# Kernel optimization log

Measured on AMD Instinct MI355X. Metric: run time of the kernel, lower is better.

Reference implementation:

```python
import jax, jax.numpy as jnp
import numpy as np

NUM_ITERS = 3
NUM_CAPSULES = 10
NUM_ROUTES = 1152  # 32*6*6
IN_CH = 16
OUT_CH = 32
BATCH = 128


def _squash(t):
    # Faithful to original squash(tensor) with default dim=1 (the batch axis here).
    n2 = jnp.sum(t * t, axis=1, keepdims=True)
    return (n2 / (1.0 + n2)) * t / jnp.sqrt(n2)


def setup_inputs() -> dict:
    key = jax.random.key(0)
    k1, k2 = jax.random.split(key)
    x = jax.random.normal(k1, (BATCH, NUM_ROUTES, IN_CH), dtype=jnp.float32)
    route_weights = jax.random.normal(
        k2, (NUM_CAPSULES, NUM_ROUTES, IN_CH, OUT_CH), dtype=jnp.float32)
    return {"x": x, "route_weights": route_weights}


def reference(x, route_weights):
    # prediction vectors u_hat: [C, B, R, O]
    pred = jnp.einsum('bri,crio->cbro', x, route_weights)
    logits = jnp.zeros_like(pred)  # [C, B, R, O], matching torch zeros of pred size
    outputs = None
    for i in range(NUM_ITERS):
        # routing_softmax with dim=2 -> softmax over the routes axis
        c = jax.nn.softmax(logits, axis=2)
        s = jnp.sum(c * pred, axis=2, keepdims=True)  # [C, B, 1, O]
        outputs = _squash(s)
        if i != NUM_ITERS - 1:
            # delta logits: [C, B, R, 1], broadcasts over O when added
            logits = logits + jnp.sum(pred * outputs, axis=-1, keepdims=True)
    # match torch output shape [C, B, 1, 1, O]
    return outputs[:, :, :, None, :]
```

## Files before the change

### kernel.cpp

```cpp
#include <hip/hip_runtime.h>
#include <math.h>

#define NB 128
#define NR 1152
#define NC 10
#define NCHK 24

typedef __attribute__((ext_vector_type(8))) short bf16x8;
typedef __attribute__((ext_vector_type(16))) float f32x16;

__device__ __forceinline__ unsigned pk_bf16(float a, float b) {
    unsigned r;
    asm("v_cvt_pk_bf16_f32 %0, %1, %2" : "=v"(r) : "v"(a), "v"(b));
    return r;
}

template<int MODE>
__global__ __launch_bounds__(512, 2) void pass_g(const float* __restrict__ x,
                                                 const float* __restrict__ W,
                                                 const float* __restrict__ oacc,
                                                 float* __restrict__ part_s,
                                                 float* __restrict__ pZ)
{
    __shared__ float lds[16384];
    const int pb = blockIdx.x;
    const int lin = (pb & 7) * 30 + (pb >> 3);
    const int rch = lin / 10;
    const int c   = lin - rch * 10;
    const int t = threadIdx.x;
    const int w = t >> 6, l = t & 63;
    const int h = w >> 1, bp = w & 1;
    const int lo5 = l & 31, hi1 = l >> 5;
    const int r0 = rch * 48 + h * 12;

    if (MODE == 1) {
        const float* ob = oacc + (size_t)c * NB * 32;
        for (int idx = t; idx < 4096; idx += 512)
            lds[(idx >> 5) * 33 + (idx & 31)] = ob[idx];
    }
    __syncthreads();

    float ov0[16], ov1[16];
    if (MODE == 1) {
#pragma unroll
        for (int j = 0; j < 16; ++j) {
            int orow = (j & 3) + 8 * (j >> 2) + 4 * hi1;
            ov0[j] = lds[(bp * 64 + lo5) * 33 + orow];
            ov1[j] = lds[(bp * 64 + 32 + lo5) * 33 + orow];
        }
    }

    f32x16 acc0, acc1, zz;
#pragma unroll
    for (int j = 0; j < 16; ++j) { acc0[j] = 0.f; acc1[j] = 0.f; zz[j] = 0.f; }
    float Z0 = 0.f, Z1 = 0.f;

    const float* wb  = W + ((size_t)(c * NR + r0) * 16 + hi1 * 8) * 32 + lo5;
    const float* xp0 = x + ((size_t)(bp * 64 + lo5) * NR + r0) * 16 + hi1 * 8;
    const float* xp1 = x + ((size_t)(bp * 64 + 32 + lo5) * NR + r0) * 16 + hi1 * 8;

    for (int rr = 0; rr < 12; ++rr) {
        float wv[8];
#pragma unroll
        for (int j = 0; j < 8; ++j) wv[j] = wb[(size_t)rr * 512 + j * 32];
        union { unsigned u[4]; bf16x8 v; } Ah, Al, Xh0, Xl0, Xh1, Xl1;
#pragma unroll
        for (int j = 0; j < 4; ++j) Ah.u[j] = pk_bf16(wv[2*j], wv[2*j+1]);
#pragma unroll
        for (int j = 0; j < 4; ++j) {
            float g0 = __uint_as_float(Ah.u[j] << 16);
            float g1 = __uint_as_float(Ah.u[j] & 0xffff0000u);
            Al.u[j] = pk_bf16(wv[2*j] - g0, wv[2*j+1] - g1);
        }
        float4 u0 = *(const float4*)(xp0 + rr * 16);
        float4 u1 = *(const float4*)(xp0 + rr * 16 + 4);
        float xv0[8] = {u0.x,u0.y,u0.z,u0.w, u1.x,u1.y,u1.z,u1.w};
#pragma unroll
        for (int j = 0; j < 4; ++j) Xh0.u[j] = pk_bf16(xv0[2*j], xv0[2*j+1]);
#pragma unroll
        for (int j = 0; j < 4; ++j) {
            float g0 = __uint_as_float(Xh0.u[j] << 16);
            float g1 = __uint_as_float(Xh0.u[j] & 0xffff0000u);
            Xl0.u[j] = pk_bf16(xv0[2*j] - g0, xv0[2*j+1] - g1);
        }
        float4 v0 = *(const float4*)(xp1 + rr * 16);
        float4 v1 = *(const float4*)(xp1 + rr * 16 + 4);
        float xv1[8] = {v0.x,v0.y,v0.z,v0.w, v1.x,v1.y,v1.z,v1.w};
#pragma unroll
        for (int j = 0; j < 4; ++j) Xh1.u[j] = pk_bf16(xv1[2*j], xv1[2*j+1]);
#pragma unroll
        for (int j = 0; j < 4; ++j) {
            float g0 = __uint_as_float(Xh1.u[j] << 16);
            float g1 = __uint_as_float(Xh1.u[j] & 0xffff0000u);
            Xl1.u[j] = pk_bf16(xv1[2*j] - g0, xv1[2*j+1] - g1);
        }

        if (MODE == 0) {
            acc0 = __builtin_amdgcn_mfma_f32_32x32x16_bf16(Ah.v, Xh0.v, acc0, 0, 0, 0);
            acc0 = __builtin_amdgcn_mfma_f32_32x32x16_bf16(Al.v, Xh0.v, acc0, 0, 0, 0);
            acc0 = __builtin_amdgcn_mfma_f32_32x32x16_bf16(Ah.v, Xl0.v, acc0, 0, 0, 0);
            acc1 = __builtin_amdgcn_mfma_f32_32x32x16_bf16(Ah.v, Xh1.v, acc1, 0, 0, 0);
            acc1 = __builtin_amdgcn_mfma_f32_32x32x16_bf16(Al.v, Xh1.v, acc1, 0, 0, 0);
            acc1 = __builtin_amdgcn_mfma_f32_32x32x16_bf16(Ah.v, Xl1.v, acc1, 0, 0, 0);
        } else {
            f32x16 q0, q1;
            q0 = __builtin_amdgcn_mfma_f32_32x32x16_bf16(Ah.v, Xh0.v, zz, 0, 0, 0);
            q1 = __builtin_amdgcn_mfma_f32_32x32x16_bf16(Ah.v, Xh1.v, zz, 0, 0, 0);
            q0 = __builtin_amdgcn_mfma_f32_32x32x16_bf16(Al.v, Xh0.v, q0, 0, 0, 0);
            q1 = __builtin_amdgcn_mfma_f32_32x32x16_bf16(Al.v, Xh1.v, q1, 0, 0, 0);
            q0 = __builtin_amdgcn_mfma_f32_32x32x16_bf16(Ah.v, Xl0.v, q0, 0, 0, 0);
            q1 = __builtin_amdgcn_mfma_f32_32x32x16_bf16(Ah.v, Xl1.v, q1, 0, 0, 0);
            float d0 = 0.f, d1 = 0.f;
#pragma unroll
            for (int j = 0; j < 16; ++j) {
                d0 = fmaf(q0[j], ov0[j], d0);
                d1 = fmaf(q1[j], ov1[j], d1);
            }
            d0 += __shfl_xor(d0, 32);
            d1 += __shfl_xor(d1, 32);
            float e0 = __expf(d0 - 20.0f);
            float e1 = __expf(d1 - 20.0f);
            Z0 += e0; Z1 += e1;
#pragma unroll
            for (int j = 0; j < 16; ++j) {
                acc0[j] = fmaf(e0, q0[j], acc0[j]);
                acc1[j] = fmaf(e1, q1[j], acc1[j]);
            }
        }
    }

    const int b0 = bp * 64 + lo5, b1 = b0 + 32;
    __syncthreads();
#pragma unroll
    for (int j = 0; j < 16; ++j) {
        int orow = (j & 3) + 8 * (j >> 2) + 4 * hi1;
        lds[h * 4096 + b0 * 32 + (orow ^ lo5)] = acc0[j];
        lds[h * 4096 + b1 * 32 + (orow ^ lo5)] = acc1[j];
    }
    __syncthreads();
    float* po = part_s + (size_t)(c * NCHK + rch) * 4096;
    for (int idx = t; idx < 4096; idx += 512) {
        int b = idx >> 5, o = idx & 31;
        float s = 0.f;
#pragma unroll
        for (int hh = 0; hh < 4; ++hh)
            s += lds[hh * 4096 + b * 32 + (o ^ (b & 31))];
        po[idx] = s;
    }
    if (MODE == 1) {
        __syncthreads();
        if (l < 32) {
            lds[h * 128 + bp * 64 + lo5] = Z0;
            lds[h * 128 + bp * 64 + 32 + lo5] = Z1;
        }
        __syncthreads();
        if (t < 128) {
            float z = lds[t] + lds[128 + t] + lds[256 + t] + lds[384 + t];
            pZ[(size_t)(c * NCHK + rch) * 128 + t] = z;
        }
    }
}

template<int MODE>
__global__ __launch_bounds__(256) void msq_k(const float* __restrict__ part_s,
                                             const float* __restrict__ pZ,
                                             float* __restrict__ oacc,
                                             float* __restrict__ dout)
{
    const int c = blockIdx.x, og = blockIdx.y;
    const int t = threadIdx.x;
    const int o_off = t & 7, b_lo = t >> 3;
    const int o = og * 8 + o_off;

    float sv[4];
    float pn = 0.f;
#pragma unroll
    for (int k = 0; k < 4; ++k) {
        int bb = b_lo + 32 * k;
        float s = 0.f;
#pragma unroll
        for (int ch = 0; ch < NCHK; ++ch)
            s += part_s[(((size_t)c * NCHK + ch) * NB + bb) * 32 + o];
        if (MODE == 0) {
            sv[k] = s * (1.0f / 1152.0f);
        } else {
            float z = 0.f;
#pragma unroll
            for (int ch = 0; ch < NCHK; ++ch)
                z += pZ[((size_t)c * NCHK + ch) * NB + bb];
            sv[k] = s / z;
        }
        pn = fmaf(sv[k], sv[k], pn);
    }
    __shared__ float red[256];
    __shared__ float fsh[8];
    red[t] = pn;
    __syncthreads();
    if (t < 8) {
        float n2 = 0.f;
#pragma unroll
        for (int j = 0; j < 32; ++j) n2 += red[t + 8 * j];
        fsh[t] = sqrtf(n2) / (1.0f + n2);
    }
    __syncthreads();
    float f = fsh[o_off];
#pragma unroll
    for (int k = 0; k < 4; ++k) {
        int bb = b_lo + 32 * k;
        float v = sv[k] * f;
        size_t idx = ((size_t)c * NB + bb) * 32 + o;
        if (MODE == 0) oacc[idx] = v;
        if (MODE == 1) oacc[idx] += v;
        if (MODE == 2) dout[idx] = v;
    }
}

extern "C" void kernel_launch(void* const* d_in, const int* in_sizes, int n_in,
                              void* d_out, int out_size, void* d_ws, size_t ws_size,
                              hipStream_t stream)
{
    (void)in_sizes; (void)n_in; (void)out_size; (void)ws_size;
    const float* x = (const float*)d_in[0];
    const float* W = (const float*)d_in[1];
    float* wsf  = (float*)d_ws;
    float* outf = (float*)d_out;

    float* part_s = wsf;
    float* pZ     = wsf + (size_t)NC * NCHK * NB * 32;
    float* oacc   = pZ  + (size_t)NC * NCHK * NB;

    dim3 mg(NC, 4);
    pass_g<0><<<240, 512, 0, stream>>>(x, W, nullptr, part_s, pZ);
    msq_k<0><<<mg, 256, 0, stream>>>(part_s, pZ, oacc, nullptr);
    pass_g<1><<<240, 512, 0, stream>>>(x, W, oacc, part_s, pZ);
    msq_k<1><<<mg, 256, 0, stream>>>(part_s, pZ, oacc, nullptr);
    pass_g<1><<<240, 512, 0, stream>>>(x, W, oacc, part_s, pZ);
    msq_k<2><<<mg, 256, 0, stream>>>(part_s, pZ, oacc, outf);
}
```

Baseline: 73.35 us.

## Split routes into 48 chunks and transpose x once for coalesced reuse

The route-chunk count doubles so each block handles 24 routes instead of 48, giving 480 blocks rather than 240 for better CU occupancy, and the inner loop is fully unrolled. In the first pass the c==0 blocks also write a transposed copy of x into the workspace. Later passes read that copy with coalesced float4 loads instead of strided reads from the original layout. In exchange, the partial-sum buffers and the msq reduction double in size, and the first pass does extra writes.

```diff
diff --git a/kernel.cpp b/kernel.cpp
--- a/kernel.cpp
+++ b/kernel.cpp
@@ -4,7 +4,7 @@
 #define NB 128
 #define NR 1152
 #define NC 10
-#define NCHK 24
+#define NCHK 48
 
 typedef __attribute__((ext_vector_type(8))) short bf16x8;
 typedef __attribute__((ext_vector_type(16))) float f32x16;
@@ -16,22 +16,23 @@
 }
 
 template<int MODE>
-__global__ __launch_bounds__(512, 2) void pass_g(const float* __restrict__ x,
+__global__ __launch_bounds__(512, 2) void pass_h(const float* __restrict__ x,
                                                  const float* __restrict__ W,
+                                                 float* __restrict__ xT,
                                                  const float* __restrict__ oacc,
-                                                 float* __restrict__ part_s,
-                                                 float* __restrict__ pZ)
+                                                 float* __restrict__ ps,
+                                                 float* __restrict__ pz)
 {
     __shared__ float lds[16384];
     const int pb = blockIdx.x;
-    const int lin = (pb & 7) * 30 + (pb >> 3);
+    const int lin = (pb & 7) * 60 + (pb >> 3);
     const int rch = lin / 10;
     const int c   = lin - rch * 10;
     const int t = threadIdx.x;
     const int w = t >> 6, l = t & 63;
     const int h = w >> 1, bp = w & 1;
     const int lo5 = l & 31, hi1 = l >> 5;
-    const int r0 = rch * 48 + h * 12;
+    const int r0 = rch * 24 + h * 6;
 
     if (MODE == 1) {
         const float* ob = oacc + (size_t)c * NB * 32;
@@ -55,14 +56,19 @@
     for (int j = 0; j < 16; ++j) { acc0[j] = 0.f; acc1[j] = 0.f; zz[j] = 0.f; }
     float Z0 = 0.f, Z1 = 0.f;
 
-    const float* wb  = W + ((size_t)(c * NR + r0) * 16 + hi1 * 8) * 32 + lo5;
+    const float* wb = W + ((size_t)(c * NR + r0) * 16 + hi1 * 8) * 32 + lo5;
     const float* xp0 = x + ((size_t)(bp * 64 + lo5) * NR + r0) * 16 + hi1 * 8;
     const float* xp1 = x + ((size_t)(bp * 64 + 32 + lo5) * NR + r0) * 16 + hi1 * 8;
-
-    for (int rr = 0; rr < 12; ++rr) {
+    float4*       xt4 = (float4*)xT;
+    const float4* xt0 = (const float4*)xT + ((size_t)(r0 * 2 + hi1) * 2) * 128 + (bp * 64 + lo5);
+    const float4* xt1 = xt0 + 32;
+    const bool wrx = (MODE == 0) && (c == 0);
+
+#pragma unroll
+    for (int rr = 0; rr < 6; ++rr) {
         float wv[8];
 #pragma unroll
-        for (int j = 0; j < 8; ++j) wv[j] = wb[(size_t)rr * 512 + j * 32];
+        for (int j = 0; j < 8; ++j) wv[j] = wb[rr * 512 + j * 32];
         union { unsigned u[4]; bf16x8 v; } Ah, Al, Xh0, Xl0, Xh1, Xl1;
 #pragma unroll
         for (int j = 0; j < 4; ++j) Ah.u[j] = pk_bf16(wv[2*j], wv[2*j+1]);
@@ -72,9 +78,27 @@
             float g1 = __uint_as_float(Ah.u[j] & 0xffff0000u);
             Al.u[j] = pk_bf16(wv[2*j] - g0, wv[2*j+1] - g1);
         }
-        float4 u0 = *(const float4*)(xp0 + rr * 16);
-        float4 u1 = *(const float4*)(xp0 + rr * 16 + 4);
+        float4 u0, u1, v0, v1;
+        if (MODE == 0) {
+            u0 = *(const float4*)(xp0 + rr * 16);
+            u1 = *(const float4*)(xp0 + rr * 16 + 4);
+            v0 = *(const float4*)(xp1 + rr * 16);
+            v1 = *(const float4*)(xp1 + rr * 16 + 4);
+            if (wrx) {
+                size_t base = ((size_t)((r0 + rr) * 2 + hi1) * 2) * 128;
+                xt4[base + (bp * 64 + lo5)]            = u0;
+                xt4[base + 128 + (bp * 64 + lo5)]      = u1;
+                xt4[base + (bp * 64 + 32 + lo5)]       = v0;
+                xt4[base + 128 + (bp * 64 + 32 + lo5)] = v1;
+            }
+        } else {
+            u0 = xt0[rr * 512];
+            u1 = xt0[rr * 512 + 128];
+            v0 = xt1[rr * 512];
+            v1 = xt1[rr * 512 + 128];
+        }
         float xv0[8] = {u0.x,u0.y,u0.z,u0.w, u1.x,u1.y,u1.z,u1.w};
+        float xv1[8] = {v0.x,v0.y,v0.z,v0.w, v1.x,v1.y,v1.z,v1.w};
 #pragma unroll
         for (int j = 0; j < 4; ++j) Xh0.u[j] = pk_bf16(xv0[2*j], xv0[2*j+1]);
 #pragma unroll
@@ -83,9 +107,6 @@
             float g1 = __uint_as_float(Xh0.u[j] & 0xffff0000u);
             Xl0.u[j] = pk_bf16(xv0[2*j] - g0, xv0[2*j+1] - g1);
         }
-        float4 v0 = *(const float4*)(xp1 + rr * 16);
-        float4 v1 = *(const float4*)(xp1 + rr * 16 + 4);
-        float xv1[8] = {v0.x,v0.y,v0.z,v0.w, v1.x,v1.y,v1.z,v1.w};
 #pragma unroll
         for (int j = 0; j < 4; ++j) Xh1.u[j] = pk_bf16(xv1[2*j], xv1[2*j+1]);
 #pragma unroll
@@ -138,7 +159,7 @@
         lds[h * 4096 + b1 * 32 + (orow ^ lo5)] = acc1[j];
     }
     __syncthreads();
-    float* po = part_s + (size_t)(c * NCHK + rch) * 4096;
+    float* po = ps + (size_t)(c * NCHK + rch) * 4096;
     for (int idx = t; idx < 4096; idx += 512) {
         int b = idx >> 5, o = idx & 31;
         float s = 0.f;
@@ -156,7 +177,7 @@
         __syncthreads();
         if (t < 128) {
             float z = lds[t] + lds[128 + t] + lds[256 + t] + lds[384 + t];
-            pZ[(size_t)(c * NCHK + rch) * 128 + t] = z;
+            pz[(size_t)(c * NCHK + rch) * 128 + t] = z;
         }
     }
 }
@@ -225,15 +246,16 @@
     float* wsf  = (float*)d_ws;
     float* outf = (float*)d_out;
 
-    float* part_s = wsf;
-    float* pZ     = wsf + (size_t)NC * NCHK * NB * 32;
-    float* oacc   = pZ  + (size_t)NC * NCHK * NB;
+    float* xT   = wsf;
+    float* ps   = xT + (size_t)NR * 16 * NB;
+    float* pz   = ps + (size_t)NC * NCHK * NB * 32;
+    float* oacc = pz + (size_t)NC * NCHK * NB;
 
     dim3 mg(NC, 4);
-    pass_g<0><<<240, 512, 0, stream>>>(x, W, nullptr, part_s, pZ);
-    msq_k<0><<<mg, 256, 0, stream>>>(part_s, pZ, oacc, nullptr);
-    pass_g<1><<<240, 512, 0, stream>>>(x, W, oacc, part_s, pZ);
-    msq_k<1><<<mg, 256, 0, stream>>>(part_s, pZ, oacc, nullptr);
-    pass_g<1><<<240, 512, 0, stream>>>(x, W, oacc, part_s, pZ);
-    msq_k<2><<<mg, 256, 0, stream>>>(part_s, pZ, oacc, outf);
-}
+    pass_h<0><<<480, 512, 0, stream>>>(x, W, xT, nullptr, ps, pz);
+    msq_k<0><<<mg, 256, 0, stream>>>(ps, pz, oacc, nullptr);
+    pass_h<1><<<480, 512, 0, stream>>>(x, W, xT, oacc, ps, pz);
+    msq_k<1><<<mg, 256, 0, stream>>>(ps, pz, oacc, nullptr);
+    pass_h<1><<<480, 512, 0, stream>>>(x, W, xT, oacc, ps, pz);
+    msq_k<2><<<mg, 256, 0, stream>>>(ps, pz, oacc, outf);
+}
```

Measured after the change: 91.55 us. +24.8%, slower.

## Fuse squash reduction into pass kernel via last-block counter, cache split-bf16 x

Applied to the files above, without the earlier changes.

Removes the separate msq_k reduction kernels: each pass block atomically bumps a per-capsule counter, and the last block to finish for that capsule reduces the partial sums and Z, squashes, and writes oacc or the output. Pass 0 also stores the hi/lo bf16 split of x to workspace so later passes load it directly instead of reloading fp32 x and reconverting. The aim is to drop three kernel launches and the x conversion work, at the cost of a memset, serialized tail work in one block per capsule, and reliance on relaxed atomics with no explicit release/acquire fence for cross-block visibility.

```diff
diff --git a/kernel.cpp b/kernel.cpp
--- a/kernel.cpp
+++ b/kernel.cpp
@@ -16,13 +16,17 @@
 }
 
 template<int MODE>
-__global__ __launch_bounds__(512, 2) void pass_g(const float* __restrict__ x,
+__global__ __launch_bounds__(512, 2) void pass_y(const float* __restrict__ x,
                                                  const float* __restrict__ W,
-                                                 const float* __restrict__ oacc,
-                                                 float* __restrict__ part_s,
-                                                 float* __restrict__ pZ)
+                                                 unsigned* __restrict__ xts,
+                                                 float* __restrict__ oacc,
+                                                 float* __restrict__ dout,
+                                                 float* __restrict__ ps,
+                                                 float* __restrict__ pz,
+                                                 int* __restrict__ cnt)
 {
     __shared__ float lds[16384];
+    __shared__ int lastFlag;
     const int pb = blockIdx.x;
     const int lin = (pb & 7) * 30 + (pb >> 3);
     const int rch = lin / 10;
@@ -33,15 +37,14 @@
     const int lo5 = l & 31, hi1 = l >> 5;
     const int r0 = rch * 48 + h * 12;
 
-    if (MODE == 1) {
-        const float* ob = oacc + (size_t)c * NB * 32;
+    if (MODE >= 1) {
         for (int idx = t; idx < 4096; idx += 512)
-            lds[(idx >> 5) * 33 + (idx & 31)] = ob[idx];
+            lds[(idx >> 5) * 33 + (idx & 31)] = oacc[(size_t)c * 4096 + idx];
     }
     __syncthreads();
 
     float ov0[16], ov1[16];
-    if (MODE == 1) {
+    if (MODE >= 1) {
 #pragma unroll
         for (int j = 0; j < 16; ++j) {
             int orow = (j & 3) + 8 * (j >> 2) + 4 * hi1;
@@ -58,12 +61,15 @@
     const float* wb  = W + ((size_t)(c * NR + r0) * 16 + hi1 * 8) * 32 + lo5;
     const float* xp0 = x + ((size_t)(bp * 64 + lo5) * NR + r0) * 16 + hi1 * 8;
     const float* xp1 = x + ((size_t)(bp * 64 + 32 + lo5) * NR + r0) * 16 + hi1 * 8;
+    uint4* xt4 = (uint4*)xts;
+    const int bq0 = bp * 64 + lo5, bq1 = bq0 + 32;
 
     for (int rr = 0; rr < 12; ++rr) {
         float wv[8];
 #pragma unroll
         for (int j = 0; j < 8; ++j) wv[j] = wb[(size_t)rr * 512 + j * 32];
-        union { unsigned u[4]; bf16x8 v; } Ah, Al, Xh0, Xl0, Xh1, Xl1;
+        union U { uint4 q; unsigned u[4]; bf16x8 v; };
+        U Ah, Al, Xh0, Xl0, Xh1, Xl1;
 #pragma unroll
         for (int j = 0; j < 4; ++j) Ah.u[j] = pk_bf16(wv[2*j], wv[2*j+1]);
 #pragma unroll
@@ -72,27 +78,41 @@
             float g1 = __uint_as_float(Ah.u[j] & 0xffff0000u);
             Al.u[j] = pk_bf16(wv[2*j] - g0, wv[2*j+1] - g1);
         }
-        float4 u0 = *(const float4*)(xp0 + rr * 16);
-        float4 u1 = *(const float4*)(xp0 + rr * 16 + 4);
-        float xv0[8] = {u0.x,u0.y,u0.z,u0.w, u1.x,u1.y,u1.z,u1.w};
-#pragma unroll
-        for (int j = 0; j < 4; ++j) Xh0.u[j] = pk_bf16(xv0[2*j], xv0[2*j+1]);
-#pragma unroll
-        for (int j = 0; j < 4; ++j) {
-            float g0 = __uint_as_float(Xh0.u[j] << 16);
-            float g1 = __uint_as_float(Xh0.u[j] & 0xffff0000u);
-            Xl0.u[j] = pk_bf16(xv0[2*j] - g0, xv0[2*j+1] - g1);
-        }
-        float4 v0 = *(const float4*)(xp1 + rr * 16);
-        float4 v1 = *(const float4*)(xp1 + rr * 16 + 4);
-        float xv1[8] = {v0.x,v0.y,v0.z,v0.w, v1.x,v1.y,v1.z,v1.w};
-#pragma unroll
-        for (int j = 0; j < 4; ++j) Xh1.u[j] = pk_bf16(xv1[2*j], xv1[2*j+1]);
-#pragma unroll
-        for (int j = 0; j < 4; ++j) {
-            float g0 = __uint_as_float(Xh1.u[j] << 16);
-            float g1 = __uint_as_float(Xh1.u[j] & 0xffff0000u);
-            Xl1.u[j] = pk_bf16(xv1[2*j] - g0, xv1[2*j+1] - g1);
+        const size_t rb4 = ((size_t)((r0 + rr) * 2 + hi1) * 2) * 128;
+        if (MODE == 0) {
+            float4 u0 = *(const float4*)(xp0 + rr * 16);
+            float4 u1 = *(const float4*)(xp0 + rr * 16 + 4);
+            float4 v0 = *(const float4*)(xp1 + rr * 16);
+            float4 v1 = *(const float4*)(xp1 + rr * 16 + 4);
+            float xv0[8] = {u0.x,u0.y,u0.z,u0.w, u1.x,u1.y,u1.z,u1.w};
+            float xv1[8] = {v0.x,v0.y,v0.z,v0.w, v1.x,v1.y,v1.z,v1.w};
+#pragma unroll
+            for (int j = 0; j < 4; ++j) Xh0.u[j] = pk_bf16(xv0[2*j], xv0[2*j+1]);
+#pragma unroll
+            for (int j = 0; j < 4; ++j) {
+                float g0 = __uint_as_float(Xh0.u[j] << 16);
+                float g1 = __uint_as_float(Xh0.u[j] & 0xffff0000u);
+                Xl0.u[j] = pk_bf16(xv0[2*j] - g0, xv0[2*j+1] - g1);
+            }
+#pragma unroll
+            for (int j = 0; j < 4; ++j) Xh1.u[j] = pk_bf16(xv1[2*j], xv1[2*j+1]);
+#pragma unroll
+            for (int j = 0; j < 4; ++j) {
+                float g0 = __uint_as_float(Xh1.u[j] << 16);
+                float g1 = __uint_as_float(Xh1.u[j] & 0xffff0000u);
+                Xl1.u[j] = pk_bf16(xv1[2*j] - g0, xv1[2*j+1] - g1);
+            }
+            if (((h * 12 + rr) % 10) == c) {
+                xt4[rb4 + bq0]       = Xh0.q;
+                xt4[rb4 + 128 + bq0] = Xl0.q;
+                xt4[rb4 + bq1]       = Xh1.q;
+                xt4[rb4 + 128 + bq1] = Xl1.q;
+            }
+        } else {
+            Xh0.q = xt4[rb4 + bq0];
+            Xl0.q = xt4[rb4 + 128 + bq0];
+            Xh1.q = xt4[rb4 + bq1];
+            Xl1.q = xt4[rb4 + 128 + bq1];
         }
 
         if (MODE == 0) {
@@ -138,16 +158,16 @@
         lds[h * 4096 + b1 * 32 + (orow ^ lo5)] = acc1[j];
     }
     __syncthreads();
-    float* po = part_s + (size_t)(c * NCHK + rch) * 4096;
+    float* po = ps + (size_t)(c * NCHK + rch) * 4096;
     for (int idx = t; idx < 4096; idx += 512) {
         int b = idx >> 5, o = idx & 31;
         float s = 0.f;
 #pragma unroll
         for (int hh = 0; hh < 4; ++hh)
             s += lds[hh * 4096 + b * 32 + (o ^ (b & 31))];
-        po[idx] = s;
-    }
-    if (MODE == 1) {
+        __hip_atomic_store(po + idx, s, __ATOMIC_RELAXED, __HIP_MEMORY_SCOPE_AGENT);
+    }
+    if (MODE >= 1) {
         __syncthreads();
         if (l < 32) {
             lds[h * 128 + bp * 64 + lo5] = Z0;
@@ -156,62 +176,63 @@
         __syncthreads();
         if (t < 128) {
             float z = lds[t] + lds[128 + t] + lds[256 + t] + lds[384 + t];
-            pZ[(size_t)(c * NCHK + rch) * 128 + t] = z;
-        }
-    }
-}
-
-template<int MODE>
-__global__ __launch_bounds__(256) void msq_k(const float* __restrict__ part_s,
-                                             const float* __restrict__ pZ,
-                                             float* __restrict__ oacc,
-                                             float* __restrict__ dout)
-{
-    const int c = blockIdx.x, og = blockIdx.y;
-    const int t = threadIdx.x;
-    const int o_off = t & 7, b_lo = t >> 3;
-    const int o = og * 8 + o_off;
-
-    float sv[4];
+            __hip_atomic_store(pz + (size_t)(c * NCHK + rch) * 128 + t, z,
+                               __ATOMIC_RELAXED, __HIP_MEMORY_SCOPE_AGENT);
+        }
+    }
+
+    __syncthreads();
+    if (t == 0) {
+        int old = __hip_atomic_fetch_add(&cnt[MODE * NC + c], 1,
+                                         __ATOMIC_RELAXED, __HIP_MEMORY_SCOPE_AGENT);
+        lastFlag = (old == NCHK - 1) ? 1 : 0;
+    }
+    __syncthreads();
+    if (!lastFlag) return;
+
+    if (MODE >= 1) {
+        if (t < NB) {
+            float z = 0.f;
+#pragma unroll
+            for (int ch = 0; ch < NCHK; ++ch)
+                z += __hip_atomic_load(pz + (size_t)(c * NCHK + ch) * 128 + t,
+                                       __ATOMIC_RELAXED, __HIP_MEMORY_SCOPE_AGENT);
+            lds[8192 + t] = z;
+        }
+        __syncthreads();
+    }
+    float sv[8];
     float pn = 0.f;
-#pragma unroll
-    for (int k = 0; k < 4; ++k) {
-        int bb = b_lo + 32 * k;
+    float* pc = ps + (size_t)c * NCHK * 4096;
+#pragma unroll
+    for (int k = 0; k < 8; ++k) {
+        int idx = t + 512 * k;
         float s = 0.f;
 #pragma unroll
         for (int ch = 0; ch < NCHK; ++ch)
-            s += part_s[(((size_t)c * NCHK + ch) * NB + bb) * 32 + o];
-        if (MODE == 0) {
-            sv[k] = s * (1.0f / 1152.0f);
-        } else {
-            float z = 0.f;
-#pragma unroll
-            for (int ch = 0; ch < NCHK; ++ch)
-                z += pZ[((size_t)c * NCHK + ch) * NB + bb];
-            sv[k] = s / z;
-        }
-        pn = fmaf(sv[k], sv[k], pn);
-    }
-    __shared__ float red[256];
-    __shared__ float fsh[8];
-    red[t] = pn;
-    __syncthreads();
-    if (t < 8) {
+            s += __hip_atomic_load(pc + (size_t)ch * 4096 + idx,
+                                   __ATOMIC_RELAXED, __HIP_MEMORY_SCOPE_AGENT);
+        float v = (MODE == 0) ? s * (1.0f / 1152.0f) : s / lds[8192 + (idx >> 5)];
+        sv[k] = v;
+        pn = fmaf(v, v, pn);
+    }
+    lds[(t >> 5) * 33 + (t & 31)] = pn;
+    __syncthreads();
+    if (t < 32) {
         float n2 = 0.f;
 #pragma unroll
-        for (int j = 0; j < 32; ++j) n2 += red[t + 8 * j];
-        fsh[t] = sqrtf(n2) / (1.0f + n2);
-    }
-    __syncthreads();
-    float f = fsh[o_off];
-#pragma unroll
-    for (int k = 0; k < 4; ++k) {
-        int bb = b_lo + 32 * k;
-        float v = sv[k] * f;
-        size_t idx = ((size_t)c * NB + bb) * 32 + o;
-        if (MODE == 0) oacc[idx] = v;
-        if (MODE == 1) oacc[idx] += v;
-        if (MODE == 2) dout[idx] = v;
+        for (int m = 0; m < 16; ++m) n2 += lds[m * 33 + t];
+        lds[1024 + t] = sqrtf(n2) / (1.0f + n2);
+    }
+    __syncthreads();
+    const float ff = lds[1024 + (t & 31)];
+#pragma unroll
+    for (int k = 0; k < 8; ++k) {
+        int idx = t + 512 * k;
+        float v = sv[k] * ff;
+        if (MODE == 0)      oacc[(size_t)c * 4096 + idx] = v;
+        else if (MODE == 1) oacc[(size_t)c * 4096 + idx] += v;
+        else                dout[(size_t)c * 4096 + idx] = v;
     }
 }
 
@@ -225,15 +246,15 @@
     float* wsf  = (float*)d_ws;
     float* outf = (float*)d_out;
 
-    float* part_s = wsf;
-    float* pZ     = wsf + (size_t)NC * NCHK * NB * 32;
-    float* oacc   = pZ  + (size_t)NC * NCHK * NB;
-
-    dim3 mg(NC, 4);
-    pass_g<0><<<240, 512, 0, stream>>>(x, W, nullptr, part_s, pZ);
-    msq_k<0><<<mg, 256, 0, stream>>>(part_s, pZ, oacc, nullptr);
-    pass_g<1><<<240, 512, 0, stream>>>(x, W, oacc, part_s, pZ);
-    msq_k<1><<<mg, 256, 0, stream>>>(part_s, pZ, oacc, nullptr);
-    pass_g<1><<<240, 512, 0, stream>>>(x, W, oacc, part_s, pZ);
-    msq_k<2><<<mg, 256, 0, stream>>>(part_s, pZ, oacc, outf);
+    unsigned* xts = (unsigned*)d_ws;
+    float* ps   = wsf + 2359296;
+    float* pz   = ps + 983040;
+    float* oacc = pz + 30720;
+    int*   cnt  = (int*)(oacc + 40960);
+
+    hipMemsetAsync(cnt, 0, 3 * NC * sizeof(int), stream);
+
+    pass_y<0><<<240, 512, 0, stream>>>(x, W, xts, oacc, nullptr, ps, pz, cnt);
+    pass_y<1><<<240, 512, 0, stream>>>(x, W, xts, oacc, nullptr, ps, pz, cnt);
+    pass_y<2><<<240, 512, 0, stream>>>(x, W, xts, oacc, outf, ps, pz, cnt);
 }
```

Result: slower. 77.56 us (+5.7%).
